# Optimization experiments

Measured on AMD Instinct MI355X. Metric: run time of the kernel, lower is better.

The kernel has to match this reference:

```python
import jax, jax.numpy as jnp
import numpy as np

V, E, H = 32000, 256, 512  # vocab, embedding_dim, hidden_size
B, S, T = 32, 64, 64       # batch, src_len, trg_len


def gru_step(h, x, W_ih, W_hh, b_ih, b_hh):
    # torch nn.GRU cell math; W_ih: [3H,E], W_hh: [3H,H], gate order r,z,n
    gi = x @ W_ih.T + b_ih        # [B,3H]
    gh = h @ W_hh.T + b_hh        # [B,3H]
    i_r, i_z, i_n = jnp.split(gi, 3, axis=-1)
    h_r, h_z, h_n = jnp.split(gh, 3, axis=-1)
    r = jax.nn.sigmoid(i_r + h_r)
    z = jax.nn.sigmoid(i_z + h_z)
    n = jnp.tanh(i_n + r * h_n)
    return (1.0 - z) * n + z * h


def setup_inputs() -> dict:
    key = jax.random.key(0)
    ks = jax.random.split(key, 16)
    u = lambda k, shape: jax.random.uniform(k, shape, jnp.float32, -0.1, 0.1)
    return {
        "src": jax.random.randint(ks[0], (B, S), 0, V),
        "trg": jax.random.randint(ks[1], (B, T), 0, V),
        "emb_enc": u(ks[2], (V, E)),
        "W_ih_enc": u(ks[3], (3 * H, E)),
        "W_hh_enc": u(ks[4], (3 * H, H)),
        "b_ih_enc": u(ks[5], (3 * H,)),
        "b_hh_enc": u(ks[6], (3 * H,)),
        "emb_dec": u(ks[7], (V, E)),
        "W_ih_dec": u(ks[8], (3 * H, E)),
        "W_hh_dec": u(ks[9], (3 * H, H)),
        "b_ih_dec": u(ks[10], (3 * H,)),
        "b_hh_dec": u(ks[11], (3 * H,)),
        "fc_W": u(ks[12], (V, H)),
        "fc_b": u(ks[13], (V,)),
    }


def reference(src, trg, emb_enc, W_ih_enc, W_hh_enc, b_ih_enc, b_hh_enc,
              emb_dec, W_ih_dec, W_hh_dec, b_ih_dec, b_hh_dec, fc_W, fc_b):
    # ----- Encoder: embed src, run GRU over time, return final hidden -----
    x_emb = emb_enc[src]                       # [B,S,E]
    h0 = jnp.zeros((B, H), jnp.float32)

    def enc_step(h, x_t):
        return gru_step(h, x_t, W_ih_enc, W_hh_enc, b_ih_enc, b_hh_enc), None

    h_enc, _ = jax.lax.scan(enc_step, h0, x_emb.transpose(1, 0, 2))  # [B,H]

    # ----- Decoder: teacher_forcing_ratio=1.0 -> inputs are trg[:, :-1] -----
    dec_in = emb_dec[trg[:, :-1]]              # [B,T-1,E]

    def dec_step(h, x_t):
        h2 = gru_step(h, x_t, W_ih_dec, W_hh_dec, b_ih_dec, b_hh_dec)
        logits = h2 @ fc_W.T + fc_b            # [B,V]
        return h2, logits

    _, logits = jax.lax.scan(dec_step, h_enc, dec_in.transpose(1, 0, 2))  # [T-1,B,V]

    # outputs[:, 0] stays zeros as in the original torch loop (range starts at 1)
    outputs = jnp.concatenate(
        [jnp.zeros((B, 1, V), jnp.float32), logits.transpose(1, 0, 2)], axis=1)
    return outputs
```

## Files before the change

### kernel.cpp

```cpp
#include <hip/hip_runtime.h>
#include <stdint.h>

constexpr int NB = 32, NS = 64, NT = 64, NV = 32000, NE = 256, NH = 512;
constexpr int RG = 64;
constexpr int UW = 16;
constexpr int BW = 16;
constexpr int GRW = 3 * UW;
constexpr int TSTEPS = NS + NT - 1;

typedef unsigned short u16;
typedef unsigned u32;
typedef short bf16x8 __attribute__((ext_vector_type(8)));
typedef float f32x4  __attribute__((ext_vector_type(4)));
typedef unsigned u32x4 __attribute__((ext_vector_type(4)));

__device__ inline u16 f2bf(float f){
  unsigned int u = __float_as_uint(f);
  u = u + 0x7FFFu + ((u >> 16) & 1u);
  return (u16)(u >> 16);
}
__device__ inline float bf2f(u16 h){ return __uint_as_float(((unsigned)h) << 16); }

__device__ inline void gload_lds16(const u16* g, u16* l){
  __builtin_amdgcn_global_load_lds((const __attribute__((address_space(1))) void*)g,
                                   (__attribute__((address_space(3))) void*)l, 16, 0, 0);
}

__device__ inline int ldsW_off(int r, int k16){
  return (k16 >> 2) * 3072 + ((r >> 4) << 10) + (((((k16 & 3) << 4)) | (r & 15)) << 4);
}
__device__ inline int ldsH_off(int r, int k16){
  int base = ((k16 >> 2) << 10) + (((((k16 & 3) << 4)) | r) << 4);
  return base ^ (((base >> 10) & 15) << 4);
}

__global__ void zero_init(float* __restrict__ out, u16* __restrict__ xdecpad, u16* __restrict__ hallpad,
                          u32* __restrict__ Hpk, u32* __restrict__ flags){
  int i = blockIdx.x * blockDim.x + threadIdx.x, st = gridDim.x * blockDim.x;
  for (int idx = i; idx < NB * NV; idx += st){
    int b = idx / NV, v = idx - b * NV;
    out[(size_t)b * NT * NV + v] = 0.f;
  }
  for (int idx = i; idx < 32 * NE; idx += st) xdecpad[idx] = 0;
  for (int idx = i; idx < 32 * NH; idx += st) hallpad[idx] = 0;
  for (int idx = i; idx < 2 * 2 * 32 * 256; idx += st) Hpk[idx] = 0;
  for (int idx = i; idx < 1024; idx += st) flags[idx] = 0;
}

__global__ void cvt_f32_bf16(const float* __restrict__ in, u16* __restrict__ out, int n4){
  int i = blockIdx.x * blockDim.x + threadIdx.x, st = gridDim.x * blockDim.x;
  for (int idx = i; idx < n4; idx += st){
    float4 v = ((const float4*)in)[idx];
    unsigned lo = (unsigned)f2bf(v.x) | ((unsigned)f2bf(v.y) << 16);
    unsigned hi = (unsigned)f2bf(v.z) | ((unsigned)f2bf(v.w) << 16);
    *(uint2*)(out + (size_t)idx * 4) = make_uint2(lo, hi);
  }
}

__global__ void cvt_hilo(const float* __restrict__ in, u16* __restrict__ hi, u16* __restrict__ lo, int n){
  int i = blockIdx.x * blockDim.x + threadIdx.x, st = gridDim.x * blockDim.x;
  for (int idx = i; idx < n; idx += st){
    float w = in[idx];
    u16 h = f2bf(w);
    hi[idx] = h;
    lo[idx] = f2bf(w - bf2f(h));
  }
}

__global__ void embed_k(const int* __restrict__ idx, int ld, int tcount,
                        const float* __restrict__ emb, u16* __restrict__ xbf){
  int tid = blockIdx.x * blockDim.x + threadIdx.x;
  int n4 = tcount * NB * (NE / 4);
  if (tid >= n4) return;
  int e4 = tid & (NE/4 - 1);
  int m  = tid >> 6;
  int t = m / NB, b = m % NB;
  int row = idx[b * ld + t];
  float4 v = ((const float4*)(emb + (size_t)row * NE))[e4];
  unsigned lo = (unsigned)f2bf(v.x) | ((unsigned)f2bf(v.y) << 16);
  unsigned hi = (unsigned)f2bf(v.z) | ((unsigned)f2bf(v.w) << 16);
  *(uint2*)(xbf + (size_t)m * NE + e4 * 4) = make_uint2(lo, hi);
}

template<int KDIM, int MODE>
__global__ __launch_bounds__(256) void gemm_bt(const u16* __restrict__ A,
                                               const u16* __restrict__ Bm,
                                               const float* __restrict__ bias,
                                               float* __restrict__ C,
                                               int Mstore, int Nld)
{
  __shared__ u16 As[2 * 128 * 32];
  __shared__ u16 Bs[2 * 128 * 32];
  const int id = blockIdx.x;
  const int q = gridDim.x >> 3;
  const int wg = (id & 7) * q + (id >> 3);
  const int m0 = (wg & 15) * 128, n0 = (wg >> 4) * 128;
  const int tid  = threadIdx.x;
  const int lane = tid & 63;
  const int w = tid >> 6, wm = w >> 1, wn = w & 1;
  f32x4 acc[4][4] = {};

  const int sr = w * 16 + (lane >> 2);
  const int sc = (lane & 3) * 8;
  const u16* aS = A  + (size_t)(m0 + sr) * KDIM + sc;
  const u16* bS = Bm + (size_t)(n0 + sr) * KDIM + sc;
  u16* asl = As + w * 16 * 32;
  u16* bsl = Bs + w * 16 * 32;

  auto STAGE = [&](int p, int k0){
    u16* ad = asl + p * 4096;
    u16* bd = bsl + p * 4096;
    gload_lds16(aS + k0, ad);
    gload_lds16(aS + (size_t)64 * KDIM + k0, ad + 64 * 32);
    gload_lds16(bS + k0, bd);
    gload_lds16(bS + (size_t)64 * KDIM + k0, bd + 64 * 32);
  };

  constexpr int NK = KDIM / 32;
  STAGE(0, 0);
  __syncthreads();
  for (int t2 = 0; t2 < NK; ++t2){
    if (t2 + 1 < NK) STAGE((t2 + 1) & 1, (t2 + 1) * 32);
    const char* Ab = (const char*)As + (t2 & 1) * 8192;
    const char* Bb = (const char*)Bs + (t2 & 1) * 8192;
    bf16x8 af[4], bfr[4];
    #pragma unroll
    for (int i = 0; i < 4; ++i)
      af[i] = *(const bf16x8*)(Ab + (wm*64 + i*16 + (lane & 15)) * 64 + (lane >> 4) * 16);
    #pragma unroll
    for (int j = 0; j < 4; ++j)
      bfr[j] = *(const bf16x8*)(Bb + (wn*64 + j*16 + (lane & 15)) * 64 + (lane >> 4) * 16);
    #pragma unroll
    for (int i = 0; i < 4; ++i)
      #pragma unroll
      for (int j = 0; j < 4; ++j)
        acc[i][j] = __builtin_amdgcn_mfma_f32_16x16x32_bf16(af[i], bfr[j], acc[i][j], 0, 0, 0);
    __syncthreads();
  }

  #pragma unroll
  for (int i = 0; i < 4; ++i){
    #pragma unroll
    for (int j = 0; j < 4; ++j){
      int col = n0 + wn*64 + j*16 + (lane & 15);
      float bv = bias[col];
      #pragma unroll
      for (int rr = 0; rr < 4; ++rr){
        int row = m0 + wm*64 + i*16 + (lane >> 4) * 4 + rr;
        float val = acc[i][j][rr] + bv;
        if (MODE == 1){
          if (row < Mstore){
            int t_ = row >> 5, b_ = row & 31;
            C[(size_t)b_ * (NT * NV) + (size_t)(t_ + 1) * NV + col] = val;
          }
        } else {
          C[(size_t)row * Nld + col] = val;
        }
      }
    }
  }
}

__global__ __launch_bounds__(256) void gru_rec(
    const u16* __restrict__ WhiE, const u16* __restrict__ WloE,
    const u16* __restrict__ WhiD, const u16* __restrict__ WloD,
    const float* __restrict__ bhhE, const float* __restrict__ bhhD,
    const float* __restrict__ gie, const float* __restrict__ gid,
    u32* __restrict__ Hpk,
    u32* __restrict__ flags,
    u16* __restrict__ Hall)
{
  extern __shared__ char smem[];
  u16* Whi = (u16*)smem;
  u16* Wlo = Whi + GRW * NH;
  u16* Hhi = Wlo + GRW * NH;
  u16* Hlo = Hhi + BW * NH;
  float* GH = (float*)(Hlo + BW * NH);

  const int tid  = threadIdx.x;
  const int lane = tid & 63;
  const int w    = tid >> 6;
  const int bg   = blockIdx.x >> 5;
  const int ug   = blockIdx.x & 31;
  const int j0   = ug * UW;
  const int b0   = bg * BW;
  const unsigned myid = blockIdx.x;

  const int gu = tid & 15, gb2 = tid >> 4;
  const int jg = j0 + gu;
  const int bglob = b0 + gb2;
  const float beR = bhhE[jg], beZ = bhhE[NH + jg], beN = bhhE[2*NH + jg];
  const float bdR = bhhD[jg], bdZ = bhhD[NH + jg], bdN = bhhD[2*NH + jg];

  auto stageW = [&](const u16* Hi, const u16* Lo){
    for (int c = tid; c < GRW * 64; c += 256){
      int r = c >> 6, k16 = c & 63;
      int grow = (r >> 4) * NH + j0 + (r & 15);
      int d = ldsW_off(r, k16);
      *(uint4*)((char*)Whi + d) = *(const uint4*)(Hi + (size_t)grow * NH + k16 * 8);
      *(uint4*)((char*)Wlo + d) = *(const uint4*)(Lo + (size_t)grow * NH + k16 * 8);
    }
  };
  stageW(WhiE, WloE);

  for (int t = 0; t < TSTEPS; ++t){
    const bool dec = (t >= NS);
    __syncthreads();
    if (tid == 0 && t > 0)
      __hip_atomic_store(&flags[myid * 4], (u32)t, __ATOMIC_RELAXED, __HIP_MEMORY_SCOPE_AGENT);
    if (t == NS) stageW(WhiD, WloD);

    {
      const u32* Hq = Hpk + (size_t)((t & 1) * 2 + bg) * 8192;
      u32x4 v[8] = {};
      unsigned have = 0;
      int spins = 0;
      const int fb = (bg << 5) + (w << 3);
      while (have != 0xffu){
        u32 f = __hip_atomic_load(&flags[(fb + (lane & 7)) * 4], __ATOMIC_RELAXED, __HIP_MEMORY_SCOPE_AGENT);
        bool rl = (lane < 8) && ((w * 8 + lane == ug) || f >= (u32)t);
        unsigned rdy = (unsigned)__ballot((int)rl) & 0xffu;
        unsigned newly = rdy & ~have;
        if (newly){
          #pragma unroll
          for (int p = 0; p < 8; ++p){
            if (newly & (1u << p)){
              const u32* src = Hq + ((w * 8 + p) << 8) + lane * 4;
              asm volatile("global_load_dwordx4 %0, %1, off sc0 sc1"
                           : "=v"(v[p]) : "v"(src) : "memory");
            }
          }
          have |= newly;
        }
        if (have != 0xffu){
          __builtin_amdgcn_s_sleep(1);
          if (++spins > (1 << 18)) break;
        }
      }
      asm volatile("s_waitcnt vmcnt(0)" ::: "memory");
      __builtin_amdgcn_sched_barrier(0);
      const int prow = lane >> 2, pq = lane & 3;
      #pragma unroll
      for (int p = 0; p < 8; ++p){
        u32 a0 = v[p][0], a1 = v[p][1], a2 = v[p][2], a3 = v[p][3];
        uint2 hw = make_uint2((a0 & 0xffffu) | (a1 << 16), (a2 & 0xffffu) | (a3 << 16));
        uint2 lw = make_uint2((a0 >> 16) | (a1 & 0xffff0000u), (a2 >> 16) | (a3 & 0xffff0000u));
        int k16 = (w * 8 + p) * 2 + (pq >> 1);
        int d = ldsH_off(prow, k16) + (pq & 1) * 8;
        *(uint2*)((char*)Hhi + d) = hw;
        *(uint2*)((char*)Hlo + d) = lw;
      }
    }
    __syncthreads();

    const float* gp = (dec ? (gid + ((size_t)(t - NS) * NB + bglob) * 1536)
                           : (gie + ((size_t)t * NB + bglob) * 1536));
    float gr = gp[jg], gz = gp[NH + jg], gn = gp[2 * NH + jg];

    if (w < 3){
      f32x4 acc0 = {0.f,0.f,0.f,0.f}, acc1 = {0.f,0.f,0.f,0.f};
      const int ab = w * 1024 + lane * 16;
      const int bb = lane * 16;
      #pragma unroll
      for (int kk = 0; kk < 16; kk += 2){
        const int bx0 = kk * 1024 + (bb ^ ((kk & 15) << 4));
        const int bx1 = (kk+1) * 1024 + (bb ^ (((kk+1) & 15) << 4));
        bf16x8 ah0 = *(const bf16x8*)((const char*)Whi + kk * 3072 + ab);
        bf16x8 al0 = *(const bf16x8*)((const char*)Wlo + kk * 3072 + ab);
        bf16x8 bh0 = *(const bf16x8*)((const char*)Hhi + bx0);
        bf16x8 bl0 = *(const bf16x8*)((const char*)Hlo + bx0);
        acc0 = __builtin_amdgcn_mfma_f32_16x16x32_bf16(ah0, bh0, acc0, 0, 0, 0);
        acc0 = __builtin_amdgcn_mfma_f32_16x16x32_bf16(al0, bh0, acc0, 0, 0, 0);
        acc0 = __builtin_amdgcn_mfma_f32_16x16x32_bf16(ah0, bl0, acc0, 0, 0, 0);
        bf16x8 ah1 = *(const bf16x8*)((const char*)Whi + (kk+1) * 3072 + ab);
        bf16x8 al1 = *(const bf16x8*)((const char*)Wlo + (kk+1) * 3072 + ab);
        bf16x8 bh1 = *(const bf16x8*)((const char*)Hhi + bx1);
        bf16x8 bl1 = *(const bf16x8*)((const char*)Hlo + bx1);
        acc1 = __builtin_amdgcn_mfma_f32_16x16x32_bf16(ah1, bh1, acc1, 0, 0, 0);
        acc1 = __builtin_amdgcn_mfma_f32_16x16x32_bf16(al1, bh1, acc1, 0, 0, 0);
        acc1 = __builtin_amdgcn_mfma_f32_16x16x32_bf16(ah1, bl1, acc1, 0, 0, 0);
      }
      f32x4 accs = acc0 + acc1;
      int col = lane & 15;
      #pragma unroll
      for (int r2 = 0; r2 < 4; ++r2){
        int row = w * 16 + ((lane >> 4) << 2) + r2;
        GH[row * 17 + col] = accs[r2];
      }
    }
    __syncthreads();

    {
      float ghr = GH[(0 * UW + gu) * 17 + gb2] + (dec ? bdR : beR);
      float ghz = GH[(1 * UW + gu) * 17 + gb2] + (dec ? bdZ : beZ);
      float ghn = GH[(2 * UW + gu) * 17 + gb2] + (dec ? bdN : beN);
      float r = 1.f / (1.f + expf(-(gr + ghr)));
      float z = 1.f / (1.f + expf(-(gz + ghz)));
      float n = tanhf(gn + r * ghn);
      int coff = ldsH_off(gb2, jg >> 3) + (jg & 7) * 2;
      float hp = bf2f(*(const u16*)((char*)Hhi + coff))
               + bf2f(*(const u16*)((char*)Hlo + coff));
      float hnew = (1.f - z) * n + z * hp;
      u16 hi = f2bf(hnew);
      u16 lo = f2bf(hnew - bf2f(hi));
      if (dec) Hall[((size_t)(t - NS) * NB + bglob) * NH + jg] = hi;
      if (t < TSTEPS - 1){
        u32* dst = Hpk + (size_t)((((t + 1) & 1) * 2 + bg) * 32 + ug) * 256 + gb2 * 16 + gu;
        __hip_atomic_store(dst, (u32)hi | ((u32)lo << 16),
                           __ATOMIC_RELAXED, __HIP_MEMORY_SCOPE_AGENT);
      }
    }
  }
}

extern "C" void kernel_launch(void* const* d_in, const int* in_sizes, int n_in,
                              void* d_out, int out_size, void* d_ws, size_t ws_size,
                              hipStream_t stream)
{
  const int*   src      = (const int*)  d_in[0];
  const int*   trg      = (const int*)  d_in[1];
  const float* emb_enc  = (const float*)d_in[2];
  const float* W_ih_enc = (const float*)d_in[3];
  const float* W_hh_enc = (const float*)d_in[4];
  const float* b_ih_enc = (const float*)d_in[5];
  const float* b_hh_enc = (const float*)d_in[6];
  const float* emb_dec  = (const float*)d_in[7];
  const float* W_ih_dec = (const float*)d_in[8];
  const float* W_hh_dec = (const float*)d_in[9];
  const float* b_ih_dec = (const float*)d_in[10];
  const float* b_hh_dec = (const float*)d_in[11];
  const float* fc_W     = (const float*)d_in[12];
  const float* fc_b     = (const float*)d_in[13];
  float* out = (float*)d_out;

  char* ws = (char*)d_ws;
  size_t o = 0;
  auto alloc = [&](size_t bytes){ size_t r = o; o += (bytes + 255) & ~(size_t)255; return r; };
  u16*   xenc  = (u16*)(ws + alloc((size_t)2048 * NE * 2));
  u16*   xdec  = (u16*)(ws + alloc((size_t)2048 * NE * 2));
  u16*   wihe  = (u16*)(ws + alloc((size_t)3 * NH * NE * 2));
  u16*   wihd  = (u16*)(ws + alloc((size_t)3 * NH * NE * 2));
  u16*   fcWbf = (u16*)(ws + alloc((size_t)NV * NH * 2));
  u16*   whiE  = (u16*)(ws + alloc((size_t)3 * NH * NH * 2));
  u16*   wloE  = (u16*)(ws + alloc((size_t)3 * NH * NH * 2));
  u16*   whiD  = (u16*)(ws + alloc((size_t)3 * NH * NH * 2));
  u16*   wloD  = (u16*)(ws + alloc((size_t)3 * NH * NH * 2));
  float* gie   = (float*)(ws + alloc((size_t)2048 * 3 * NH * 4));
  float* gid   = (float*)(ws + alloc((size_t)2048 * 3 * NH * 4));
  u32*   Hpk   = (u32*)(ws + alloc((size_t)2 * 2 * 32 * 256 * 4));
  u32*   flags = (u32*)(ws + alloc(4096));
  u16*   Hall  = (u16*)(ws + alloc((size_t)2048 * NH * 2));

  zero_init<<<256, 256, 0, stream>>>(out, xdec + (size_t)2016 * NE, Hall + (size_t)2016 * NH, Hpk, flags);
  cvt_f32_bf16<<<384, 256, 0, stream>>>(W_ih_enc, wihe, 3*NH*NE/4);
  cvt_f32_bf16<<<384, 256, 0, stream>>>(W_ih_dec, wihd, 3*NH*NE/4);
  cvt_f32_bf16<<<2048, 256, 0, stream>>>(fc_W, fcWbf, NV*NH/4);
  cvt_hilo<<<1024, 256, 0, stream>>>(W_hh_enc, whiE, wloE, 3*NH*NH);
  cvt_hilo<<<1024, 256, 0, stream>>>(W_hh_dec, whiD, wloD, 3*NH*NH);
  embed_k<<<(NS*NB*64 + 255)/256, 256, 0, stream>>>(src, NS, NS, emb_enc, xenc);
  embed_k<<<((NT-1)*NB*64 + 255)/256, 256, 0, stream>>>(trg, NT, NT-1, emb_dec, xdec);

  gemm_bt<NE, 0><<<192, 256, 0, stream>>>(xenc, wihe, b_ih_enc, gie, 2048, 3*NH);
  gemm_bt<NE, 0><<<192, 256, 0, stream>>>(xdec, wihd, b_ih_dec, gid, 2048, 3*NH);

  constexpr int SMEM_BYTES = 2 * (GRW * NH * 2) + 2 * (BW * NH * 2) + GRW * 17 * 4;
  static_assert(SMEM_BYTES <= 160 * 1024, "LDS over 160 KiB");
  static_assert(SMEM_BYTES == 134336, "unexpected LDS size");
  (void)hipFuncSetAttribute(reinterpret_cast<const void*>(&gru_rec),
                            hipFuncAttributeMaxDynamicSharedMemorySize, SMEM_BYTES);
  gru_rec<<<RG, 256, SMEM_BYTES, stream>>>(whiE, wloE, whiD, wloD, b_hh_enc, b_hh_dec,
                                           gie, gid, Hpk, flags, Hall);

  gemm_bt<NH, 1><<<4000, 256, 0, stream>>>(Hall, fcWbf, fc_b, out, 2016, 0);
}
```

Baseline: 626.0 us.

## Fuse output projection GEMM into recurrent kernel as flag-gated worker blocks

The separate FC logits GEMM launch is folded into the GRU recurrence kernel. 192 extra worker blocks wait on per-block progress flags and start each 128-row chunk of decoder hidden states as soon as the recurrence has produced it, so the large projection overlaps the serial decoder steps. Hidden states are now published as 32-bit atomic stores. The flag poll is simplified to wait on all flags before issuing a batched load. Risks include worker blocks competing with recurrence blocks for CUs, the higher LDS footprint, and reliance on all blocks being co-resident, since workers spin-wait on the recurrence blocks.

```diff
diff --git a/kernel.cpp b/kernel.cpp
--- a/kernel.cpp
+++ b/kernel.cpp
@@ -7,6 +7,7 @@
 constexpr int BW = 16;
 constexpr int GRW = 3 * UW;
 constexpr int TSTEPS = NS + NT - 1;
+constexpr int NWK = 192;
 
 typedef unsigned short u16;
 typedef unsigned u32;
@@ -34,7 +35,41 @@
   return base ^ (((base >> 10) & 15) << 4);
 }
 
-__global__ void zero_init(float* __restrict__ out, u16* __restrict__ xdecpad, u16* __restrict__ hallpad,
+__device__ inline void load_h128(const u32* p, u32x4 v[8]){
+  asm volatile(
+    "global_load_dwordx4 %0, %8, off sc0 sc1\n\t"
+    "global_load_dwordx4 %1, %8, off offset:16 sc0 sc1\n\t"
+    "global_load_dwordx4 %2, %8, off offset:32 sc0 sc1\n\t"
+    "global_load_dwordx4 %3, %8, off offset:48 sc0 sc1\n\t"
+    "global_load_dwordx4 %4, %8, off offset:64 sc0 sc1\n\t"
+    "global_load_dwordx4 %5, %8, off offset:80 sc0 sc1\n\t"
+    "global_load_dwordx4 %6, %8, off offset:96 sc0 sc1\n\t"
+    "global_load_dwordx4 %7, %8, off offset:112 sc0 sc1\n\t"
+    "s_waitcnt vmcnt(0)"
+    : "=&v"(v[0]), "=&v"(v[1]), "=&v"(v[2]), "=&v"(v[3]),
+      "=&v"(v[4]), "=&v"(v[5]), "=&v"(v[6]), "=&v"(v[7])
+    : "v"(p)
+    : "memory");
+}
+
+__device__ inline void load8blk(const u32* p0, const u32* p1, u32x4 v[8]){
+  asm volatile(
+    "global_load_dwordx4 %0, %8, off sc0 sc1\n\t"
+    "global_load_dwordx4 %1, %8, off offset:1024 sc0 sc1\n\t"
+    "global_load_dwordx4 %2, %8, off offset:2048 sc0 sc1\n\t"
+    "global_load_dwordx4 %3, %8, off offset:3072 sc0 sc1\n\t"
+    "global_load_dwordx4 %4, %9, off sc0 sc1\n\t"
+    "global_load_dwordx4 %5, %9, off offset:1024 sc0 sc1\n\t"
+    "global_load_dwordx4 %6, %9, off offset:2048 sc0 sc1\n\t"
+    "global_load_dwordx4 %7, %9, off offset:3072 sc0 sc1\n\t"
+    "s_waitcnt vmcnt(0)"
+    : "=&v"(v[0]), "=&v"(v[1]), "=&v"(v[2]), "=&v"(v[3]),
+      "=&v"(v[4]), "=&v"(v[5]), "=&v"(v[6]), "=&v"(v[7])
+    : "v"(p0), "v"(p1)
+    : "memory");
+}
+
+__global__ void zero_init(float* __restrict__ out, u16* __restrict__ xdecpad, u32* __restrict__ hcpad,
                           u32* __restrict__ Hpk, u32* __restrict__ flags){
   int i = blockIdx.x * blockDim.x + threadIdx.x, st = gridDim.x * blockDim.x;
   for (int idx = i; idx < NB * NV; idx += st){
@@ -42,7 +77,7 @@
     out[(size_t)b * NT * NV + v] = 0.f;
   }
   for (int idx = i; idx < 32 * NE; idx += st) xdecpad[idx] = 0;
-  for (int idx = i; idx < 32 * NH; idx += st) hallpad[idx] = 0;
+  for (int idx = i; idx < 32 * NH; idx += st) hcpad[idx] = 0;
   for (int idx = i; idx < 2 * 2 * 32 * 256; idx += st) Hpk[idx] = 0;
   for (int idx = i; idx < 1024; idx += st) flags[idx] = 0;
 }
@@ -82,12 +117,11 @@
   *(uint2*)(xbf + (size_t)m * NE + e4 * 4) = make_uint2(lo, hi);
 }
 
-template<int KDIM, int MODE>
+template<int KDIM>
 __global__ __launch_bounds__(256) void gemm_bt(const u16* __restrict__ A,
                                                const u16* __restrict__ Bm,
                                                const float* __restrict__ bias,
-                                               float* __restrict__ C,
-                                               int Mstore, int Nld)
+                                               float* __restrict__ C, int Nld)
 {
   __shared__ u16 As[2 * 128 * 32];
   __shared__ u16 Bs[2 * 128 * 32];
@@ -147,167 +181,252 @@
       #pragma unroll
       for (int rr = 0; rr < 4; ++rr){
         int row = m0 + wm*64 + i*16 + (lane >> 4) * 4 + rr;
-        float val = acc[i][j][rr] + bv;
-        if (MODE == 1){
-          if (row < Mstore){
-            int t_ = row >> 5, b_ = row & 31;
-            C[(size_t)b_ * (NT * NV) + (size_t)(t_ + 1) * NV + col] = val;
-          }
-        } else {
-          C[(size_t)row * Nld + col] = val;
-        }
+        C[(size_t)row * Nld + col] = acc[i][j][rr] + bv;
       }
     }
   }
 }
 
-__global__ __launch_bounds__(256) void gru_rec(
+__global__ __launch_bounds__(256) void gru_fused(
     const u16* __restrict__ WhiE, const u16* __restrict__ WloE,
     const u16* __restrict__ WhiD, const u16* __restrict__ WloD,
     const float* __restrict__ bhhE, const float* __restrict__ bhhD,
     const float* __restrict__ gie, const float* __restrict__ gid,
     u32* __restrict__ Hpk,
     u32* __restrict__ flags,
-    u16* __restrict__ Hall)
+    u32* __restrict__ HallC,
+    const u16* __restrict__ fcWbf, const float* __restrict__ fc_b,
+    float* __restrict__ out)
 {
   extern __shared__ char smem[];
-  u16* Whi = (u16*)smem;
-  u16* Wlo = Whi + GRW * NH;
-  u16* Hhi = Wlo + GRW * NH;
-  u16* Hlo = Hhi + BW * NH;
-  float* GH = (float*)(Hlo + BW * NH);
-
   const int tid  = threadIdx.x;
   const int lane = tid & 63;
   const int w    = tid >> 6;
-  const int bg   = blockIdx.x >> 5;
-  const int ug   = blockIdx.x & 31;
-  const int j0   = ug * UW;
-  const int b0   = bg * BW;
-  const unsigned myid = blockIdx.x;
-
-  const int gu = tid & 15, gb2 = tid >> 4;
-  const int jg = j0 + gu;
-  const int bglob = b0 + gb2;
-  const float beR = bhhE[jg], beZ = bhhE[NH + jg], beN = bhhE[2*NH + jg];
-  const float bdR = bhhD[jg], bdZ = bhhD[NH + jg], bdN = bhhD[2*NH + jg];
-
-  auto stageW = [&](const u16* Hi, const u16* Lo){
-    for (int c = tid; c < GRW * 64; c += 256){
-      int r = c >> 6, k16 = c & 63;
-      int grow = (r >> 4) * NH + j0 + (r & 15);
-      int d = ldsW_off(r, k16);
-      *(uint4*)((char*)Whi + d) = *(const uint4*)(Hi + (size_t)grow * NH + k16 * 8);
-      *(uint4*)((char*)Wlo + d) = *(const uint4*)(Lo + (size_t)grow * NH + k16 * 8);
+
+  if (blockIdx.x < RG){
+    u16* Whi = (u16*)smem;
+    u16* Wlo = Whi + GRW * NH;
+    u16* Hhi = Wlo + GRW * NH;
+    u16* Hlo = Hhi + BW * NH;
+    float* GH = (float*)(Hlo + BW * NH);
+
+    const int bg   = blockIdx.x >> 5;
+    const int ug   = blockIdx.x & 31;
+    const int j0   = ug * UW;
+    const int b0   = bg * BW;
+    const unsigned myid = blockIdx.x;
+
+    const int gu = tid & 15, gb2 = tid >> 4;
+    const int jg = j0 + gu;
+    const int bglob = b0 + gb2;
+    const float beR = bhhE[jg], beZ = bhhE[NH + jg], beN = bhhE[2*NH + jg];
+    const float bdR = bhhD[jg], bdZ = bhhD[NH + jg], bdN = bhhD[2*NH + jg];
+
+    auto stageW = [&](const u16* Hi, const u16* Lo){
+      for (int c = tid; c < GRW * 64; c += 256){
+        int r = c >> 6, k16 = c & 63;
+        int grow = (r >> 4) * NH + j0 + (r & 15);
+        int d = ldsW_off(r, k16);
+        *(uint4*)((char*)Whi + d) = *(const uint4*)(Hi + (size_t)grow * NH + k16 * 8);
+        *(uint4*)((char*)Wlo + d) = *(const uint4*)(Lo + (size_t)grow * NH + k16 * 8);
+      }
+    };
+    stageW(WhiE, WloE);
+
+    for (int t = 0; t < TSTEPS; ++t){
+      const bool dec = (t >= NS);
+      __syncthreads();
+      if (tid == 0 && t > 0)
+        __hip_atomic_store(&flags[myid * 4], (u32)t, __ATOMIC_RELAXED, __HIP_MEMORY_SCOPE_AGENT);
+      if (t == NS) stageW(WhiD, WloD);
+
+      {
+        const u32* Hq = Hpk + (size_t)((t & 1) * 2 + bg) * 8192;
+        const int fb = (bg << 5) + (w << 3);
+        int spins = 0;
+        while (true){
+          u32 f = __hip_atomic_load(&flags[(fb + (lane & 7)) * 4], __ATOMIC_RELAXED, __HIP_MEMORY_SCOPE_AGENT);
+          if (__all((int)((lane >= 8) || (w * 8 + lane == ug) || f >= (u32)t))) break;
+          __builtin_amdgcn_s_sleep(1);
+          if (++spins > (1 << 18)) break;
+        }
+        u32x4 v[8];
+        const u32* p0 = Hq + ((w * 8 + 0) << 8) + lane * 4;
+        const u32* p1 = Hq + ((w * 8 + 4) << 8) + lane * 4;
+        load8blk(p0, p1, v);
+        __builtin_amdgcn_sched_barrier(0);
+        const int prow = lane >> 2, pq = lane & 3;
+        #pragma unroll
+        for (int p = 0; p < 8; ++p){
+          u32 a0 = v[p][0], a1 = v[p][1], a2 = v[p][2], a3 = v[p][3];
+          uint2 hw = make_uint2((a0 & 0xffffu) | (a1 << 16), (a2 & 0xffffu) | (a3 << 16));
+          uint2 lw = make_uint2((a0 >> 16) | (a1 & 0xffff0000u), (a2 >> 16) | (a3 & 0xffff0000u));
+          int k16 = (w * 8 + p) * 2 + (pq >> 1);
+          int d = ldsH_off(prow, k16) + (pq & 1) * 8;
+          *(uint2*)((char*)Hhi + d) = hw;
+          *(uint2*)((char*)Hlo + d) = lw;
+        }
+      }
+      __syncthreads();
+
+      const float* gp = (dec ? (gid + ((size_t)(t - NS) * NB + bglob) * 1536)
+                             : (gie + ((size_t)t * NB + bglob) * 1536));
+      float gr = gp[jg], gz = gp[NH + jg], gn = gp[2 * NH + jg];
+
+      if (w < 3){
+        f32x4 acc0 = {0.f,0.f,0.f,0.f}, acc1 = {0.f,0.f,0.f,0.f};
+        const int ab = w * 1024 + lane * 16;
+        const int bb = lane * 16;
+        #pragma unroll
+        for (int kk = 0; kk < 16; kk += 2){
+          const int bx0 = kk * 1024 + (bb ^ ((kk & 15) << 4));
+          const int bx1 = (kk+1) * 1024 + (bb ^ (((kk+1) & 15) << 4));
+          bf16x8 ah0 = *(const bf16x8*)((const char*)Whi + kk * 3072 + ab);
+          bf16x8 al0 = *(const bf16x8*)((const char*)Wlo + kk * 3072 + ab);
+          bf16x8 bh0 = *(const bf16x8*)((const char*)Hhi + bx0);
+          bf16x8 bl0 = *(const bf16x8*)((const char*)Hlo + bx0);
+          acc0 = __builtin_amdgcn_mfma_f32_16x16x32_bf16(ah0, bh0, acc0, 0, 0, 0);
+          acc0 = __builtin_amdgcn_mfma_f32_16x16x32_bf16(al0, bh0, acc0, 0, 0, 0);
+          acc0 = __builtin_amdgcn_mfma_f32_16x16x32_bf16(ah0, bl0, acc0, 0, 0, 0);
+          bf16x8 ah1 = *(const bf16x8*)((const char*)Whi + (kk+1) * 3072 + ab);
+          bf16x8 al1 = *(const bf16x8*)((const char*)Wlo + (kk+1) * 3072 + ab);
+          bf16x8 bh1 = *(const bf16x8*)((const char*)Hhi + bx1);
+          bf16x8 bl1 = *(const bf16x8*)((const char*)Hlo + bx1);
+          acc1 = __builtin_amdgcn_mfma_f32_16x16x32_bf16(ah1, bh1, acc1, 0, 0, 0);
+          acc1 = __builtin_amdgcn_mfma_f32_16x16x32_bf16(al1, bh1, acc1, 0, 0, 0);
+          acc1 = __builtin_amdgcn_mfma_f32_16x16x32_bf16(ah1, bl1, acc1, 0, 0, 0);
+        }
+        f32x4 accs = acc0 + acc1;
+        int col = lane & 15;
+        #pragma unroll
+        for (int r2 = 0; r2 < 4; ++r2){
+          int row = w * 16 + ((lane >> 4) << 2) + r2;
+          GH[row * 17 + col] = accs[r2];
+        }
+      }
+      __syncthreads();
+
+      {
+        float ghr = GH[(0 * UW + gu) * 17 + gb2] + (dec ? bdR : beR);
+        float ghz = GH[(1 * UW + gu) * 17 + gb2] + (dec ? bdZ : beZ);
+        float ghn = GH[(2 * UW + gu) * 17 + gb2] + (dec ? bdN : beN);
+        float r = 1.f / (1.f + expf(-(gr + ghr)));
+        float z = 1.f / (1.f + expf(-(gz + ghz)));
+        float n = tanhf(gn + r * ghn);
+        int coff = ldsH_off(gb2, jg >> 3) + (jg & 7) * 2;
+        float hp = bf2f(*(const u16*)((char*)Hhi + coff))
+                 + bf2f(*(const u16*)((char*)Hlo + coff));
+        float hnew = (1.f - z) * n + z * hp;
+        u16 hi = f2bf(hnew);
+        u16 lo = f2bf(hnew - bf2f(hi));
+        if (dec)
+          __hip_atomic_store(&HallC[((size_t)(t - NS) * NB + bglob) * NH + jg], (u32)hi,
+                             __ATOMIC_RELAXED, __HIP_MEMORY_SCOPE_AGENT);
+        if (t < TSTEPS - 1){
+          u32* dst = Hpk + (size_t)((((t + 1) & 1) * 2 + bg) * 32 + ug) * 256 + gb2 * 16 + gu;
+          __hip_atomic_store(dst, (u32)hi | ((u32)lo << 16),
+                             __ATOMIC_RELAXED, __HIP_MEMORY_SCOPE_AGENT);
+        }
+        asm volatile("s_waitcnt vmcnt(0)" ::: "memory");
+      }
     }
-  };
-  stageW(WhiE, WloE);
-
-  for (int t = 0; t < TSTEPS; ++t){
-    const bool dec = (t >= NS);
     __syncthreads();
-    if (tid == 0 && t > 0)
-      __hip_atomic_store(&flags[myid * 4], (u32)t, __ATOMIC_RELAXED, __HIP_MEMORY_SCOPE_AGENT);
-    if (t == NS) stageW(WhiD, WloD);
+    if (tid == 0)
+      __hip_atomic_store(&flags[myid * 4], 127u, __ATOMIC_RELAXED, __HIP_MEMORY_SCOPE_AGENT);
+
+  } else {
+    u16* Asm = (u16*)smem;
+    u16* Bs  = (u16*)(smem + 131072);
+
+    const int wk = blockIdx.x - RG;
+    const int g  = wk / 12;
+    const int wi = wk - g * 12;
+    const u32 need = (g == 15) ? 127u : (u32)(NS + 4 * (g + 1));
+
+    if (w == 0){
+      int spins = 0;
+      while (true){
+        u32 f = __hip_atomic_load(&flags[lane * 4], __ATOMIC_RELAXED, __HIP_MEMORY_SCOPE_AGENT);
+        if (__all((int)(f >= need))) break;
+        __builtin_amdgcn_s_sleep(8);
+        if (++spins > (1 << 20)) break;
+      }
+    }
+    __syncthreads();
 
     {
-      const u32* Hq = Hpk + (size_t)((t & 1) * 2 + bg) * 8192;
-      u32x4 v[8] = {};
-      unsigned have = 0;
-      int spins = 0;
-      const int fb = (bg << 5) + (w << 3);
-      while (have != 0xffu){
-        u32 f = __hip_atomic_load(&flags[(fb + (lane & 7)) * 4], __ATOMIC_RELAXED, __HIP_MEMORY_SCOPE_AGENT);
-        bool rl = (lane < 8) && ((w * 8 + lane == ug) || f >= (u32)t);
-        unsigned rdy = (unsigned)__ballot((int)rl) & 0xffu;
-        unsigned newly = rdy & ~have;
-        if (newly){
+      const u32* Am = HallC + (size_t)g * 128 * 512;
+      #pragma unroll
+      for (int s = 0; s < 8; ++s){
+        int seg = tid + 256 * s;
+        int row = seg >> 4;
+        u32x4 v[8];
+        load_h128(Am + (size_t)seg * 32, v);
+        __builtin_amdgcn_sched_barrier(0);
+        #pragma unroll
+        for (int j = 0; j < 8; ++j){
+          int k4 = (seg & 15) * 8 + j;
+          uint2 pk = make_uint2((v[j][0] & 0xffffu) | (v[j][1] << 16),
+                                (v[j][2] & 0xffffu) | (v[j][3] << 16));
+          *(uint2*)((char*)Asm + row * 1024 + ((k4 * 8) ^ ((row & 7) << 4))) = pk;
+        }
+      }
+    }
+    __syncthreads();
+
+    const int wm = w >> 1, wn = w & 1;
+    const int sr = w * 16 + (lane >> 2);
+    const int sc = (lane & 3) * 8;
+
+    for (int n = wi; n < 250; n += 12){
+      const int n0 = n * 128;
+      const u16* bS = fcWbf + (size_t)(n0 + sr) * NH + sc;
+      u16* bsl = Bs + w * 16 * 32;
+      f32x4 acc[4][4] = {};
+
+      gload_lds16(bS, bsl);
+      gload_lds16(bS + (size_t)64 * NH, bsl + 64 * 32);
+      __syncthreads();
+      for (int ks = 0; ks < 16; ++ks){
+        if (ks + 1 < 16){
+          u16* bd = bsl + ((ks + 1) & 1) * 4096;
+          gload_lds16(bS + (ks + 1) * 32, bd);
+          gload_lds16(bS + (size_t)64 * NH + (ks + 1) * 32, bd + 64 * 32);
+        }
+        const char* Bb = (const char*)Bs + (ks & 1) * 8192;
+        bf16x8 af[4], bfr[4];
+        #pragma unroll
+        for (int i = 0; i < 4; ++i){
+          int row = wm * 64 + i * 16 + (lane & 15);
+          af[i] = *(const bf16x8*)((const char*)Asm + row * 1024 +
+                   ((ks * 64 + (lane >> 4) * 16) ^ ((row & 7) << 4)));
+        }
+        #pragma unroll
+        for (int j = 0; j < 4; ++j)
+          bfr[j] = *(const bf16x8*)(Bb + (wn*64 + j*16 + (lane & 15)) * 64 + (lane >> 4) * 16);
+        #pragma unroll
+        for (int i = 0; i < 4; ++i)
           #pragma unroll
-          for (int p = 0; p < 8; ++p){
-            if (newly & (1u << p)){
-              const u32* src = Hq + ((w * 8 + p) << 8) + lane * 4;
-              asm volatile("global_load_dwordx4 %0, %1, off sc0 sc1"
-                           : "=v"(v[p]) : "v"(src) : "memory");
+          for (int j = 0; j < 4; ++j)
+            acc[i][j] = __builtin_amdgcn_mfma_f32_16x16x32_bf16(af[i], bfr[j], acc[i][j], 0, 0, 0);
+        __syncthreads();
+      }
+
+      #pragma unroll
+      for (int i = 0; i < 4; ++i){
+        #pragma unroll
+        for (int j = 0; j < 4; ++j){
+          int col = n0 + wn*64 + j*16 + (lane & 15);
+          float bv = fc_b[col];
+          #pragma unroll
+          for (int rr = 0; rr < 4; ++rr){
+            int row = g * 128 + wm*64 + i*16 + (lane >> 4) * 4 + rr;
+            if (row < 2016){
+              int t_ = row >> 5, b_ = row & 31;
+              out[(size_t)b_ * (NT * NV) + (size_t)(t_ + 1) * NV + col] = acc[i][j][rr] + bv;
             }
           }
-          have |= newly;
-        }
-        if (have != 0xffu){
-          __builtin_amdgcn_s_sleep(1);
-          if (++spins > (1 << 18)) break;
-        }
-      }
-      asm volatile("s_waitcnt vmcnt(0)" ::: "memory");
-      __builtin_amdgcn_sched_barrier(0);
-      const int prow = lane >> 2, pq = lane & 3;
-      #pragma unroll
-      for (int p = 0; p < 8; ++p){
-        u32 a0 = v[p][0], a1 = v[p][1], a2 = v[p][2], a3 = v[p][3];
-        uint2 hw = make_uint2((a0 & 0xffffu) | (a1 << 16), (a2 & 0xffffu) | (a3 << 16));
-        uint2 lw = make_uint2((a0 >> 16) | (a1 & 0xffff0000u), (a2 >> 16) | (a3 & 0xffff0000u));
-        int k16 = (w * 8 + p) * 2 + (pq >> 1);
-        int d = ldsH_off(prow, k16) + (pq & 1) * 8;
-        *(uint2*)((char*)Hhi + d) = hw;
-        *(uint2*)((char*)Hlo + d) = lw;
-      }
-    }
-    __syncthreads();
-
-    const float* gp = (dec ? (gid + ((size_t)(t - NS) * NB + bglob) * 1536)
-                           : (gie + ((size_t)t * NB + bglob) * 1536));
-    float gr = gp[jg], gz = gp[NH + jg], gn = gp[2 * NH + jg];
-
-    if (w < 3){
-      f32x4 acc0 = {0.f,0.f,0.f,0.f}, acc1 = {0.f,0.f,0.f,0.f};
-      const int ab = w * 1024 + lane * 16;
-      const int bb = lane * 16;
-      #pragma unroll
-      for (int kk = 0; kk < 16; kk += 2){
-        const int bx0 = kk * 1024 + (bb ^ ((kk & 15) << 4));
-        const int bx1 = (kk+1) * 1024 + (bb ^ (((kk+1) & 15) << 4));
-        bf16x8 ah0 = *(const bf16x8*)((const char*)Whi + kk * 3072 + ab);
-        bf16x8 al0 = *(const bf16x8*)((const char*)Wlo + kk * 3072 + ab);
-        bf16x8 bh0 = *(const bf16x8*)((const char*)Hhi + bx0);
-        bf16x8 bl0 = *(const bf16x8*)((const char*)Hlo + bx0);
-        acc0 = __builtin_amdgcn_mfma_f32_16x16x32_bf16(ah0, bh0, acc0, 0, 0, 0);
-        acc0 = __builtin_amdgcn_mfma_f32_16x16x32_bf16(al0, bh0, acc0, 0, 0, 0);
-        acc0 = __builtin_amdgcn_mfma_f32_16x16x32_bf16(ah0, bl0, acc0, 0, 0, 0);
-        bf16x8 ah1 = *(const bf16x8*)((const char*)Whi + (kk+1) * 3072 + ab);
-        bf16x8 al1 = *(const bf16x8*)((const char*)Wlo + (kk+1) * 3072 + ab);
-        bf16x8 bh1 = *(const bf16x8*)((const char*)Hhi + bx1);
-        bf16x8 bl1 = *(const bf16x8*)((const char*)Hlo + bx1);
-        acc1 = __builtin_amdgcn_mfma_f32_16x16x32_bf16(ah1, bh1, acc1, 0, 0, 0);
-        acc1 = __builtin_amdgcn_mfma_f32_16x16x32_bf16(al1, bh1, acc1, 0, 0, 0);
-        acc1 = __builtin_amdgcn_mfma_f32_16x16x32_bf16(ah1, bl1, acc1, 0, 0, 0);
-      }
-      f32x4 accs = acc0 + acc1;
-      int col = lane & 15;
-      #pragma unroll
-      for (int r2 = 0; r2 < 4; ++r2){
-        int row = w * 16 + ((lane >> 4) << 2) + r2;
-        GH[row * 17 + col] = accs[r2];
-      }
-    }
-    __syncthreads();
-
-    {
-      float ghr = GH[(0 * UW + gu) * 17 + gb2] + (dec ? bdR : beR);
-      float ghz = GH[(1 * UW + gu) * 17 + gb2] + (dec ? bdZ : beZ);
-      float ghn = GH[(2 * UW + gu) * 17 + gb2] + (dec ? bdN : beN);
-      float r = 1.f / (1.f + expf(-(gr + ghr)));
-      float z = 1.f / (1.f + expf(-(gz + ghz)));
-      float n = tanhf(gn + r * ghn);
-      int coff = ldsH_off(gb2, jg >> 3) + (jg & 7) * 2;
-      float hp = bf2f(*(const u16*)((char*)Hhi + coff))
-               + bf2f(*(const u16*)((char*)Hlo + coff));
-      float hnew = (1.f - z) * n + z * hp;
-      u16 hi = f2bf(hnew);
-      u16 lo = f2bf(hnew - bf2f(hi));
-      if (dec) Hall[((size_t)(t - NS) * NB + bglob) * NH + jg] = hi;
-      if (t < TSTEPS - 1){
-        u32* dst = Hpk + (size_t)((((t + 1) & 1) * 2 + bg) * 32 + ug) * 256 + gb2 * 16 + gu;
-        __hip_atomic_store(dst, (u32)hi | ((u32)lo << 16),
-                           __ATOMIC_RELAXED, __HIP_MEMORY_SCOPE_AGENT);
+        }
       }
     }
   }
@@ -349,9 +468,9 @@
   float* gid   = (float*)(ws + alloc((size_t)2048 * 3 * NH * 4));
   u32*   Hpk   = (u32*)(ws + alloc((size_t)2 * 2 * 32 * 256 * 4));
   u32*   flags = (u32*)(ws + alloc(4096));
-  u16*   Hall  = (u16*)(ws + alloc((size_t)2048 * NH * 2));
-
-  zero_init<<<256, 256, 0, stream>>>(out, xdec + (size_t)2016 * NE, Hall + (size_t)2016 * NH, Hpk, flags);
+  u32*   HallC = (u32*)(ws + alloc((size_t)2048 * NH * 4));
+
+  zero_init<<<256, 256, 0, stream>>>(out, xdec + (size_t)2016 * NE, HallC + (size_t)2016 * NH, Hpk, flags);
   cvt_f32_bf16<<<384, 256, 0, stream>>>(W_ih_enc, wihe, 3*NH*NE/4);
   cvt_f32_bf16<<<384, 256, 0, stream>>>(W_ih_dec, wihd, 3*NH*NE/4);
   cvt_f32_bf16<<<2048, 256, 0, stream>>>(fc_W, fcWbf, NV*NH/4);
@@ -360,16 +479,16 @@
   embed_k<<<(NS*NB*64 + 255)/256, 256, 0, stream>>>(src, NS, NS, emb_enc, xenc);
   embed_k<<<((NT-1)*NB*64 + 255)/256, 256, 0, stream>>>(trg, NT, NT-1, emb_dec, xdec);
 
-  gemm_bt<NE, 0><<<192, 256, 0, stream>>>(xenc, wihe, b_ih_enc, gie, 2048, 3*NH);
-  gemm_bt<NE, 0><<<192, 256, 0, stream>>>(xdec, wihd, b_ih_dec, gid, 2048, 3*NH);
-
-  constexpr int SMEM_BYTES = 2 * (GRW * NH * 2) + 2 * (BW * NH * 2) + GRW * 17 * 4;
+  gemm_bt<NE><<<192, 256, 0, stream>>>(xenc, wihe, b_ih_enc, gie, 3*NH);
+  gemm_bt<NE><<<192, 256, 0, stream>>>(xdec, wihd, b_ih_dec, gid, 3*NH);
+
+  constexpr int SMEM_REC = 2 * (GRW * NH * 2) + 2 * (BW * NH * 2) + GRW * 17 * 4;
+  constexpr int SMEM_WRK = 128 * NH * 2 + 2 * (128 * 32 * 2);
+  constexpr int SMEM_BYTES = (SMEM_REC > SMEM_WRK) ? SMEM_REC : SMEM_WRK;
   static_assert(SMEM_BYTES <= 160 * 1024, "LDS over 160 KiB");
-  static_assert(SMEM_BYTES == 134336, "unexpected LDS size");
-  (void)hipFuncSetAttribute(reinterpret_cast<const void*>(&gru_rec),
+  static_assert(SMEM_BYTES == 147456, "unexpected LDS size");
+  (void)hipFuncSetAttribute(reinterpret_cast<const void*>(&gru_fused),
                             hipFuncAttributeMaxDynamicSharedMemorySize, SMEM_BYTES);
-  gru_rec<<<RG, 256, SMEM_BYTES, stream>>>(whiE, wloE, whiD, wloD, b_hh_enc, b_hh_dec,
-                                           gie, gid, Hpk, flags, Hall);
-
-  gemm_bt<NH, 1><<<4000, 256, 0, stream>>>(Hall, fcWbf, fc_b, out, 2016, 0);
-}
+  gru_fused<<<RG + NWK, 256, SMEM_BYTES, stream>>>(whiE, wloE, whiD, wloD, b_hh_enc, b_hh_dec,
+                                                   gie, gid, Hpk, flags, HallC, fcWbf, fc_b, out);
+}
```

New measurement: 830.9 us. +32.7%, slower.
